# Optimization experiments

Measured on AMD Instinct MI355X. Metric: run time of the kernel, lower is better.

## Reference

```python
import jax, jax.numpy as jnp
import numpy as np

M, N, DIM, B = 64, 64, 512, 4096
SIGMA = max(M, N) / 2.0  # default sigma in BaseSOM.__init__


def setup_inputs() -> dict:
    key = jax.random.key(0)
    k1, k2 = jax.random.split(key)
    batch = jax.random.normal(k1, (B, DIM), dtype=jnp.float32)
    weights = jax.random.uniform(k2, (M * N, DIM), dtype=jnp.float32)
    # grid locations [(i, j) for i in range(M) for j in range(N)]
    ii, jj = jnp.meshgrid(jnp.arange(M), jnp.arange(N), indexing="ij")
    locations = jnp.stack([ii.reshape(-1), jj.reshape(-1)], axis=1).astype(jnp.int64)
    return {
        "batch": batch,
        "weights": weights,
        "locations": locations,
        "decay_rate": 1000,
        "it": 100,
    }


def reference(batch, weights, locations, decay_rate, it):
    # Squared Euclidean distances (argmin is identical to argmin of cdist p=2).
    x2 = jnp.sum(batch * batch, axis=1, keepdims=True)          # [B, 1]
    w2 = jnp.sum(weights * weights, axis=1)[None, :]            # [1, MN]
    d2 = x2 - 2.0 * (batch @ weights.T) + w2                    # [B, MN]
    bmu_indices = jnp.argmin(d2, axis=1)                        # [B]
    bmu_loc = locations[bmu_indices]                            # [B, 2]
    lr = jnp.exp(-jnp.float32(it) / jnp.float32(decay_rate))
    sigma_op = jnp.float32(SIGMA) * lr
    # [B, MN, 2] grid offsets -> squared grid distance [B, MN]
    diff = locations[None, :, :].astype(jnp.float32) - bmu_loc[:, None, :].astype(jnp.float32)
    dist_sq = jnp.sum(diff * diff, axis=2)
    return jnp.exp(-dist_sq / (sigma_op * sigma_op))
```

## Files before the change

kernel.cpp:

```cpp
#include <hip/hip_runtime.h>
#include <cfloat>

#define DIMK 512
#define MN   4096
#define BATCH 4096
#define BK 32

typedef _Float16 half8_t __attribute__((ext_vector_type(8)));
typedef float f32x4 __attribute__((ext_vector_type(4)));

#define GLD16(gp, lp) __builtin_amdgcn_global_load_lds( \
    (const __attribute__((address_space(1))) void*)(gp), \
    (__attribute__((address_space(3))) void*)(lp), 16, 0, 0)

__global__ __launch_bounds__(256) void convert_kernel(
        const float* __restrict__ X, const float* __restrict__ W,
        _Float16* __restrict__ Xh, _Float16* __restrict__ Wh,
        float* __restrict__ w2, float* __restrict__ xnorm) {
    const int blk  = blockIdx.x;
    const int t    = threadIdx.x;
    const bool isW = blk >= 1024;
    const float* src = isW ? W : X;
    _Float16* dst  = isW ? Wh : Xh;
    const int rblk = isW ? blk - 1024 : blk;
    const size_t idx = (size_t)rblk * 2048 + (size_t)t * 8;

    float4 v0 = *(const float4*)(src + idx);
    float4 v1 = *(const float4*)(src + idx + 4);
    float v[8] = {v0.x, v0.y, v0.z, v0.w, v1.x, v1.y, v1.z, v1.w};
    half8_t hv;
    float s = 0.f;
#pragma unroll
    for (int e = 0; e < 8; e++) {
        s += v[e] * v[e];
        hv[e] = (_Float16)v[e];
    }
    *(half8_t*)(dst + idx) = hv;
#pragma unroll
    for (int o = 32; o > 0; o >>= 1) s += __shfl_down(s, o);
    if ((t & 63) == 0) {
        int row = rblk * 4 + (t >> 6);
        if (isW) w2[row] = s;
        else     xnorm[row] = __fsqrt_rn(s);
    }
}

__global__ __launch_bounds__(256, 4) void score_kernel(
        const _Float16* __restrict__ Xh, const _Float16* __restrict__ Wh,
        const float* __restrict__ w2, float* __restrict__ S) {
    __shared__ __align__(16) _Float16 lds[2][8192];

    const int t    = threadIdx.x;
    const int lane = t & 63;
    const int w    = t >> 6;
    const int wm   = w >> 1;
    const int wn   = w & 1;
    const int m0   = blockIdx.y * 128;
    const int n0   = blockIdx.x * 128;

    f32x4 acc[4][4];
#pragma unroll
    for (int i = 0; i < 4; i++)
#pragma unroll
        for (int j = 0; j < 4; j++) acc[i][j] = (f32x4){0.f, 0.f, 0.f, 0.f};

    const int r16 = lane & 15;
    const int kg  = lane >> 4;
    const int b0  = 2 * w, b1 = 2 * w + 1;
    const size_t ko = (size_t)kg * 8;
    const _Float16* gA0 = Xh + (size_t)(m0 + b0 * 16 + r16) * DIMK + ko;
    const _Float16* gA1 = Xh + (size_t)(m0 + b1 * 16 + r16) * DIMK + ko;
    const _Float16* gB0 = Wh + (size_t)(n0 + b0 * 16 + r16) * DIMK + ko;
    const _Float16* gB1 = Wh + (size_t)(n0 + b1 * 16 + r16) * DIMK + ko;
    const int dA0 = b0 * 512,        dA1 = b1 * 512;
    const int dB0 = 4096 + b0 * 512, dB1 = 4096 + b1 * 512;

    GLD16(gA0, &lds[0][dA0]);
    GLD16(gA1, &lds[0][dA1]);
    GLD16(gB0, &lds[0][dB0]);
    GLD16(gB1, &lds[0][dB1]);

    int cur = 0;
    for (int k0 = 0; k0 < DIMK; k0 += BK) {
        __syncthreads();
        if (k0 + BK < DIMK) {
            int nk = k0 + BK;
            GLD16(gA0 + nk, &lds[cur ^ 1][dA0]);
            GLD16(gA1 + nk, &lds[cur ^ 1][dA1]);
            GLD16(gB0 + nk, &lds[cur ^ 1][dB0]);
            GLD16(gB1 + nk, &lds[cur ^ 1][dB1]);
        }
        const _Float16* sA = &lds[cur][0];
        const _Float16* sB = &lds[cur][4096];

        half8_t ah[4], bh[4];
#pragma unroll
        for (int i = 0; i < 4; i++) {
            ah[i] = *(const half8_t*)(sA + (wm * 4 + i) * 512 + lane * 8);
            bh[i] = *(const half8_t*)(sB + (wn * 4 + i) * 512 + lane * 8);
        }
#pragma unroll
        for (int i = 0; i < 4; i++)
#pragma unroll
            for (int j = 0; j < 4; j++)
                acc[i][j] = __builtin_amdgcn_mfma_f32_16x16x32_f16(ah[i], bh[j], acc[i][j], 0, 0, 0);
        cur ^= 1;
    }

    const int q  = lane >> 4;
    const int cl = lane & 15;
    float w2v[4];
#pragma unroll
    for (int j = 0; j < 4; j++) w2v[j] = w2[n0 + wn * 64 + j * 16 + cl];
#pragma unroll
    for (int i = 0; i < 4; i++)
#pragma unroll
        for (int v = 0; v < 4; v++) {
            int row = m0 + wm * 64 + i * 16 + q * 4 + v;
            float* Srow = S + (size_t)row * 4096 + n0 + wn * 64;
#pragma unroll
            for (int j = 0; j < 4; j++)
                Srow[j * 16 + cl] = w2v[j] - 2.0f * acc[i][j][v];
        }
}

__global__ __launch_bounds__(256) void epilogue_kernel(
        const float* __restrict__ w2, const float* __restrict__ xnorm,
        const float* __restrict__ X, const float* __restrict__ W,
        const int* __restrict__ decay_p, const int* __restrict__ it_p,
        float* out) {
    __shared__ float xs[512];
    __shared__ float wval[4];
    __shared__ int   widx[4];
    __shared__ int   list[257];
    __shared__ int   cnt;
    __shared__ float sgmin;
    __shared__ int   sgidx;
    __shared__ int   sfin;
    __shared__ float tab[128];
    const int row  = blockIdx.x;
    const int t    = threadIdx.x;
    const int lane = t & 63;
    const int w    = t >> 6;

    {
        float2 xv = *(const float2*)(X + (size_t)row * DIMK + t * 2);
        xs[2 * t]     = xv.x;
        xs[2 * t + 1] = xv.y;
    }
    if (t == 0) cnt = 0;

    const f32x4* S4 = (const f32x4*)(out + (size_t)row * 4096);
    f32x4 sv[4];
    float bv = FLT_MAX;
    int   bi = 0x7FFFFFFF;
#pragma unroll
    for (int k = 0; k < 4; k++) {
        sv[k] = S4[k * 256 + t];
#pragma unroll
        for (int e = 0; e < 4; e++) {
            int col = k * 1024 + t * 4 + e;
            if (sv[k][e] < bv) { bv = sv[k][e]; bi = col; }
        }
    }
#pragma unroll
    for (int mask = 1; mask <= 32; mask <<= 1) {
        float ov = __shfl_xor(bv, mask);
        int   oi = __shfl_xor(bi, mask);
        if (ov < bv || (ov == bv && oi < bi)) { bv = ov; bi = oi; }
    }
    if (lane == 0) { wval[w] = bv; widx[w] = bi; }
    __syncthreads();
    if (t == 0) {
        float g = wval[0]; int gi = widx[0];
#pragma unroll
        for (int k = 1; k < 4; k++)
            if (wval[k] < g || (wval[k] == g && widx[k] < gi)) { g = wval[k]; gi = widx[k]; }
        sgmin = g; sgidx = gi;
    }
    __syncthreads();

    const float tau = sgmin + 2.0f * (0.0222f * xnorm[row] + 0.1f);
#pragma unroll
    for (int k = 0; k < 4; k++)
#pragma unroll
        for (int e = 0; e < 4; e++) {
            int col = k * 1024 + t * 4 + e;
            if (sv[k][e] <= tau && col != sgidx) {
                int p = atomicAdd(&cnt, 1);
                if (p < 255) list[p] = col;
            }
        }
    __syncthreads();
    int total = cnt;
    int rr, cc;
    if (total == 0) {
        rr = sgidx >> 6; cc = sgidx & 63;
    } else {
        if (t == 0) { list[min(total, 255)] = sgidx; }
        __syncthreads();
        total = min(total, 255) + 1;
        float mbv = FLT_MAX;
        int   mbi = 0x7FFFFFFF;
        for (int idx = w; idx < total; idx += 4) {
            int col = list[idx];
            const float* wr = W + (size_t)col * DIMK;
            float p = 0.f;
#pragma unroll
            for (int e = 0; e < 8; e++) p += xs[lane * 8 + e] * wr[lane * 8 + e];
#pragma unroll
            for (int mask = 1; mask <= 32; mask <<= 1) p += __shfl_xor(p, mask);
            float s = w2[col] - 2.0f * p;
            if (s < mbv || (s == mbv && col < mbi)) { mbv = s; mbi = col; }
        }
        if (lane == 0) { wval[w] = mbv; widx[w] = mbi; }
        __syncthreads();
        if (t == 0) {
            float g = wval[0]; int gi = widx[0];
#pragma unroll
            for (int k = 1; k < 4; k++)
                if (wval[k] < g || (wval[k] == g && widx[k] < gi)) { g = wval[k]; gi = widx[k]; }
            sfin = gi;
        }
        __syncthreads();
        rr = sfin >> 6; cc = sfin & 63;
    }

    const float lr  = __expf(-(float)(*it_p) / (float)(*decay_p));
    const float so  = 32.0f * lr;
    const float inv = 1.0f / (so * so);
    if (t < 64) {
        float d = (float)(t - rr);
        tab[t] = __expf(-d * d * inv);
    } else if (t < 128) {
        float d = (float)(t - 64 - cc);
        tab[t] = __expf(-d * d * inv);
    }
    __syncthreads();
    const float* er = tab;
    const float* ec = tab + 64;
    f32x4* orow = (f32x4*)(out + (size_t)row * 4096);
#pragma unroll
    for (int qq = 0; qq < 4; qq++) {
        int f  = qq * 256 + t;
        int i  = f >> 4;
        int j0 = (f & 15) * 4;
        float e = er[i];
        f32x4 o = {e * ec[j0], e * ec[j0 + 1], e * ec[j0 + 2], e * ec[j0 + 3]};
        __builtin_nontemporal_store(o, orow + f);
    }
}

extern "C" void kernel_launch(void* const* d_in, const int* in_sizes, int n_in,
                              void* d_out, int out_size, void* d_ws, size_t ws_size,
                              hipStream_t stream) {
    const float* X       = (const float*)d_in[0];
    const float* W       = (const float*)d_in[1];
    const int*   decay_p = (const int*)d_in[3];
    const int*   it_p    = (const int*)d_in[4];
    float* out = (float*)d_out;

    _Float16* Xh = (_Float16*)d_ws;
    _Float16* Wh = Xh + (size_t)BATCH * DIMK;
    float*    w2 = (float*)(Wh + (size_t)MN * DIMK);
    float*    xn = w2 + MN;

    convert_kernel<<<2048, 256, 0, stream>>>(X, W, Xh, Wh, w2, xn);
    score_kernel<<<dim3(32, 32), 256, 0, stream>>>(Xh, Wh, w2, out);
    epilogue_kernel<<<BATCH, 256, 0, stream>>>(w2, xn, X, W, decay_p, it_p, out);
}
```

Before: 153.3 us.

## Store per-group-of-4 column minima from GEMM and refine candidates in fp32

```diff
diff --git a/kernel.cpp b/kernel.cpp
--- a/kernel.cpp
+++ b/kernel.cpp
@@ -5,6 +5,7 @@
 #define MN   4096
 #define BATCH 4096
 #define BK 32
+#define NGRP 1024
 
 typedef _Float16 half8_t __attribute__((ext_vector_type(8)));
 typedef float f32x4 __attribute__((ext_vector_type(4)));
@@ -47,7 +48,7 @@
 
 __global__ __launch_bounds__(256, 4) void score_kernel(
         const _Float16* __restrict__ Xh, const _Float16* __restrict__ Wh,
-        const float* __restrict__ w2, float* __restrict__ S) {
+        const float* __restrict__ w2, float* __restrict__ Gm ) {
     __shared__ __align__(16) _Float16 lds[2][8192];
 
     const int t    = threadIdx.x;
@@ -107,8 +108,9 @@
         cur ^= 1;
     }
 
-    const int q  = lane >> 4;
-    const int cl = lane & 15;
+    const int q   = lane >> 4;
+    const int cl  = lane & 15;
+    const int gb  = (n0 >> 2) + wn * 16;
     float w2v[4];
 #pragma unroll
     for (int j = 0; j < 4; j++) w2v[j] = w2[n0 + wn * 64 + j * 16 + cl];
@@ -116,11 +118,15 @@
     for (int i = 0; i < 4; i++)
 #pragma unroll
         for (int v = 0; v < 4; v++) {
-            int row = m0 + wm * 64 + i * 16 + q * 4 + v;
-            float* Srow = S + (size_t)row * 4096 + n0 + wn * 64;
-#pragma unroll
-            for (int j = 0; j < 4; j++)
-                Srow[j * 16 + cl] = w2v[j] - 2.0f * acc[i][j][v];
+            const int row = m0 + wm * 64 + i * 16 + q * 4 + v;
+            float* grow = Gm + (size_t)row * 4096 + gb;
+#pragma unroll
+            for (int j = 0; j < 4; j++) {
+                float s = w2v[j] - 2.0f * acc[i][j][v];
+                s = fminf(s, __shfl_xor(s, 1));
+                s = fminf(s, __shfl_xor(s, 2));
+                if ((cl & 3) == 0) grow[j * 4 + (cl >> 2)] = s;
+            }
         }
 }
 
@@ -130,13 +136,13 @@
         const int* __restrict__ decay_p, const int* __restrict__ it_p,
         float* out) {
     __shared__ float xs[512];
-    __shared__ float wval[4];
-    __shared__ int   widx[4];
-    __shared__ int   list[257];
+    __shared__ int   list[NGRP];
     __shared__ int   cnt;
-    __shared__ float sgmin;
-    __shared__ int   sgidx;
-    __shared__ int   sfin;
+    __shared__ float wmin[4];
+    __shared__ float svv[4];
+    __shared__ int   svi[4];
+    __shared__ float sbv;
+    __shared__ int   sbi;
     __shared__ float tab[128];
     const int row  = blockIdx.x;
     const int t    = threadIdx.x;
@@ -148,87 +154,51 @@
         xs[2 * t]     = xv.x;
         xs[2 * t + 1] = xv.y;
     }
-    if (t == 0) cnt = 0;
-
-    const f32x4* S4 = (const f32x4*)(out + (size_t)row * 4096);
-    f32x4 sv[4];
-    float bv = FLT_MAX;
-    int   bi = 0x7FFFFFFF;
-#pragma unroll
-    for (int k = 0; k < 4; k++) {
-        sv[k] = S4[k * 256 + t];
-#pragma unroll
-        for (int e = 0; e < 4; e++) {
-            int col = k * 1024 + t * 4 + e;
-            if (sv[k][e] < bv) { bv = sv[k][e]; bi = col; }
-        }
-    }
-#pragma unroll
-    for (int mask = 1; mask <= 32; mask <<= 1) {
-        float ov = __shfl_xor(bv, mask);
-        int   oi = __shfl_xor(bi, mask);
-        if (ov < bv || (ov == bv && oi < bi)) { bv = ov; bi = oi; }
-    }
-    if (lane == 0) { wval[w] = bv; widx[w] = bi; }
+    if (t == 0) { cnt = 0; sbv = FLT_MAX; sbi = 0x7FFFFFFF; }
+
+    f32x4 gm = *((const f32x4*)(out + (size_t)row * 4096) + t);
+    float g = fminf(fminf(gm[0], gm[1]), fminf(gm[2], gm[3]));
+#pragma unroll
+    for (int mask = 1; mask <= 32; mask <<= 1)
+        g = fminf(g, __shfl_xor(g, mask));
+    if (lane == 0) wmin[w] = g;
     __syncthreads();
-    if (t == 0) {
-        float g = wval[0]; int gi = widx[0];
-#pragma unroll
-        for (int k = 1; k < 4; k++)
-            if (wval[k] < g || (wval[k] == g && widx[k] < gi)) { g = wval[k]; gi = widx[k]; }
-        sgmin = g; sgidx = gi;
-    }
+    const float gmin = fminf(fminf(wmin[0], wmin[1]), fminf(wmin[2], wmin[3]));
+    const float tau  = gmin + 2.0f * (0.0222f * xnorm[row] + 0.1f);
+
+#pragma unroll
+    for (int e = 0; e < 4; e++)
+        if (gm[e] <= tau) list[atomicAdd(&cnt, 1)] = t * 4 + e;
     __syncthreads();
-
-    const float tau = sgmin + 2.0f * (0.0222f * xnorm[row] + 0.1f);
-#pragma unroll
-    for (int k = 0; k < 4; k++)
-#pragma unroll
-        for (int e = 0; e < 4; e++) {
-            int col = k * 1024 + t * 4 + e;
-            if (sv[k][e] <= tau && col != sgidx) {
-                int p = atomicAdd(&cnt, 1);
-                if (p < 255) list[p] = col;
-            }
-        }
-    __syncthreads();
-    int total = cnt;
-    int rr, cc;
-    if (total == 0) {
-        rr = sgidx >> 6; cc = sgidx & 63;
-    } else {
-        if (t == 0) { list[min(total, 255)] = sgidx; }
-        __syncthreads();
-        total = min(total, 255) + 1;
-        float mbv = FLT_MAX;
-        int   mbi = 0x7FFFFFFF;
-        for (int idx = w; idx < total; idx += 4) {
-            int col = list[idx];
-            const float* wr = W + (size_t)col * DIMK;
-            float p = 0.f;
-#pragma unroll
-            for (int e = 0; e < 8; e++) p += xs[lane * 8 + e] * wr[lane * 8 + e];
-#pragma unroll
-            for (int mask = 1; mask <= 32; mask <<= 1) p += __shfl_xor(p, mask);
-            float s = w2[col] - 2.0f * p;
-            if (s < mbv || (s == mbv && col < mbi)) { mbv = s; mbi = col; }
-        }
-        if (lane == 0) { wval[w] = mbv; widx[w] = mbi; }
+    const int total = cnt;
+
+    for (int idx = 0; idx < total; idx++) {
+        const int col = list[idx] * 4 + w;
+        const float* wr = W + (size_t)col * DIMK;
+        float p = 0.f;
+#pragma unroll
+        for (int e = 0; e < 8; e++) p += xs[lane * 8 + e] * wr[lane * 8 + e];
+#pragma unroll
+        for (int mask = 1; mask <= 32; mask <<= 1) p += __shfl_xor(p, mask);
+        if (lane == 0) {
+            svv[w] = w2[col] - 2.0f * p;
+            svi[w] = col;
+        }
         __syncthreads();
         if (t == 0) {
-            float g = wval[0]; int gi = widx[0];
-#pragma unroll
-            for (int k = 1; k < 4; k++)
-                if (wval[k] < g || (wval[k] == g && widx[k] < gi)) { g = wval[k]; gi = widx[k]; }
-            sfin = gi;
+#pragma unroll
+            for (int k = 0; k < 4; k++) {
+                float s = svv[k]; int c = svi[k];
+                if (s < sbv || (s == sbv && c < sbi)) { sbv = s; sbi = c; }
+            }
         }
         __syncthreads();
-        rr = sfin >> 6; cc = sfin & 63;
     }
 
     const float lr  = __expf(-(float)(*it_p) / (float)(*decay_p));
     const float so  = 32.0f * lr;
     const float inv = 1.0f / (so * so);
+    const int rr = sbi >> 6, cc = sbi & 63;
     if (t < 64) {
         float d = (float)(t - rr);
         tab[t] = __expf(-d * d * inv);
```

Result: faster. 144.8 us (-5.5%).
